# Kernel optimization log

Measured on AMD Instinct MI355X. Metric: run time of the kernel, lower is better.

## Reference

```python
import jax, jax.numpy as jnp
import numpy as np

STATE_LEN = 128
SEQ_LEN = 2048  # middle segment length; total T = SEQ_LEN + 2*STATE_LEN = 2304


def _l2norm(t):
    # matches torch F.normalize(p=2, dim=-1, eps=1e-12)
    n = jnp.sqrt(jnp.sum(t * t, axis=-1, keepdims=True))
    return t / jnp.maximum(n, 1e-12)


def setup_inputs() -> dict:
    key = jax.random.key(0)
    ks = jax.random.split(key, 8)
    B, D, H, dk, dv = 1, 1024, 16, 64, 64
    T = SEQ_LEN + 2 * STATE_LEN
    x = jax.random.normal(ks[0], (B, T, D), dtype=jnp.float32)
    w = lambda k, do: jax.random.normal(k, (H, D, do), dtype=jnp.float32) * 0.02
    return {
        "x": x,
        "Wq": w(ks[1], dk),
        "Wk": w(ks[2], dk),
        "Wv": w(ks[3], dv),
        "Wq_state": w(ks[4], dk),
        "Wk_state": w(ks[5], dk),
        "Wv_state": w(ks[6], dv),
        "scaling_factor": jnp.full((H,), 1.0 / np.sqrt(dk), dtype=jnp.float32),
    }


def reference(x, Wq, Wk, Wv, Wq_state, Wk_state, Wv_state, scaling_factor):
    sl, seq = STATE_LEN, SEQ_LEN
    # extract_state: [start_state | sequence | end_state]
    x0 = x[:, :sl]
    xm = x[:, sl:sl + seq]
    x1 = x[:, sl + seq:]

    proj = lambda t, W: jnp.einsum('bsd,hdk->bhsk', t, W)  # StackedLinear, no bias

    q = jnp.concatenate([_l2norm(proj(x0, Wq_state)), _l2norm(proj(xm, Wq)), _l2norm(proj(x1, Wq_state))], axis=2)
    k = jnp.concatenate([_l2norm(proj(x0, Wk_state)), _l2norm(proj(xm, Wk)), _l2norm(proj(x1, Wk_state))], axis=2)
    v = jnp.concatenate([_l2norm(proj(x0, Wv_state)), _l2norm(proj(xm, Wv)), _l2norm(proj(x1, Wv_state))], axis=2)

    T = q.shape[2]
    row = jnp.arange(T)[:, None]
    col = jnp.arange(T)[None, :]
    allowed = col <= row  # causal (tril, diagonal=0)
    # end-state rows may not attend to start-state cols (attn_bias[..., seq+sl:seq+2sl, :sl] = 0 before log)
    allowed = allowed & ~((row >= sl + seq) & (col < sl))
    mask = jnp.where(allowed, 0.0, -jnp.inf).astype(q.dtype)  # log of 0/1 tril

    # per-head learnable scale applied to q@k^T, then additive mask, softmax, @v
    scores = jnp.einsum('bhqd,bhkd->bhqk', q, k) * scaling_factor[None, :, None, None] + mask
    att = jax.nn.softmax(scores, axis=-1)
    return jnp.einsum('bhqk,bhkd->bhqd', att, v)
```

## Files before the change

### kernel.cpp

```cpp
#include <hip/hip_runtime.h>
#include <hip/hip_bf16.h>

#define T_TOT 2304
#define DDIM  1024
#define NH    16
#define DK    64
#define SLEN  128
#define SEQ   2048

typedef __bf16 bf16x8 __attribute__((ext_vector_type(8)));
typedef __bf16 bf16x4 __attribute__((ext_vector_type(4)));
typedef float  f32x4  __attribute__((ext_vector_type(4)));

__device__ __forceinline__ void async_copy16(const void* gsrc, void* ldst) {
  __builtin_amdgcn_global_load_lds(
      (const __attribute__((address_space(1))) void*)gsrc,
      (__attribute__((address_space(3))) void*)ldst, 16, 0, 0);
}

__global__ __launch_bounds__(256) void convert_kernel(
    const float* __restrict__ x,
    const float* __restrict__ Wq, const float* __restrict__ Wk,
    const float* __restrict__ Wv, const float* __restrict__ Wqs,
    const float* __restrict__ Wks, const float* __restrict__ Wvs,
    __bf16* __restrict__ xb, __bf16* __restrict__ Wt) {
  const int b = blockIdx.x;
  const int tid = threadIdx.x;
  if (b < 576) {
    const float4* xin = (const float4*)x;
#pragma unroll
    for (int it = 0; it < 4; ++it) {
      int idx4 = b * 1024 + it * 256 + tid;
      float4 v = xin[idx4];
      bf16x4 o;
      o[0] = (__bf16)v.x; o[1] = (__bf16)v.y; o[2] = (__bf16)v.z; o[3] = (__bf16)v.w;
      *(bf16x4*)(xb + (size_t)idx4 * 4) = o;
    }
    return;
  }
  __shared__ float tile[64 * 65];
  const int wb = b - 576;
  const int m  = wb >> 8;
  const int rem = wb & 255;
  const int h  = rem >> 4;
  const int dt = rem & 15;
  const int d0 = dt * 64;
  const float* Wsrc = (m == 0 ? Wq : m == 1 ? Wk : m == 2 ? Wv
                      : m == 3 ? Wqs : m == 4 ? Wks : Wvs) + (size_t)h * (DDIM * DK);
#pragma unroll
  for (int rr = 0; rr < 4; ++rr) {
    int drow = rr * 16 + (tid >> 4);
    int nc   = (tid & 15) * 4;
    float4 v = *(const float4*)(Wsrc + (size_t)(d0 + drow) * DK + nc);
    tile[(nc + 0) * 65 + drow] = v.x;
    tile[(nc + 1) * 65 + drow] = v.y;
    tile[(nc + 2) * 65 + drow] = v.z;
    tile[(nc + 3) * 65 + drow] = v.w;
  }
  __syncthreads();
  {
    int n  = tid >> 2;
    int rg = (tid & 3) * 16;
    __bf16* dst = Wt + (((size_t)(m * NH + h)) * DK + n) * DDIM + d0 + rg;
    bf16x8 o0, o1;
#pragma unroll
    for (int e = 0; e < 8; e++) o0[e] = (__bf16)tile[n * 65 + rg + e];
#pragma unroll
    for (int e = 0; e < 8; e++) o1[e] = (__bf16)tile[n * 65 + rg + 8 + e];
    *(bf16x8*)dst = o0;
    *(bf16x8*)(dst + 8) = o1;
  }
}

__global__ __launch_bounds__(256) void proj_kernel(
    const __bf16* __restrict__ xb, const __bf16* __restrict__ Wt,
    const float* __restrict__ scal,
    __bf16* __restrict__ qkv, __bf16* __restrict__ vt) {
  const int ntile = blockIdx.x;
  const int rt    = blockIdx.y;
  const int which = blockIdx.z;
  const int r0    = rt * 128;
  const int m     = (rt == 0 || rt == 17) ? which + 3 : which;

  __shared__ __bf16 Xs[128 * 64];
  __shared__ __bf16 Wsh[128 * 64];

  const int tid  = threadIdx.x;
  const int wave = tid >> 6, lane = tid & 63;
  const int quad = lane >> 4, lc = lane & 15;
  const int wr   = wave >> 1, wc = wave & 1;
  const int h    = ntile * 2 + wc;

  const __bf16* Wbase = Wt + ((size_t)m * NH) * (DK * DDIM) + (size_t)(ntile * 128) * DDIM;

  const f32x4 fz = {0.f, 0.f, 0.f, 0.f};
  f32x4 acc[4][4];
#pragma unroll
  for (int i = 0; i < 4; i++)
#pragma unroll
    for (int j = 0; j < 4; j++) acc[i][j] = fz;

  for (int k0 = 0; k0 < DDIM; k0 += 64) {
#pragma unroll
    for (int it = 0; it < 4; ++it) {
      int L = it * 256 + tid;
      int row = L >> 3, c = (L & 7) ^ ((L >> 3) & 7);
      async_copy16(xb + (size_t)(r0 + row) * DDIM + k0 + c * 8,
                   (char*)Xs + (size_t)(it * 256 + wave * 64) * 16);
    }
#pragma unroll
    for (int it = 0; it < 4; ++it) {
      int L = it * 256 + tid;
      int row = L >> 3, c = (L & 7) ^ ((L >> 3) & 7);
      async_copy16(Wbase + (size_t)row * DDIM + k0 + c * 8,
                   (char*)Wsh + (size_t)(it * 256 + wave * 64) * 16);
    }
    __syncthreads();
#pragma unroll
    for (int kk = 0; kk < 2; kk++) {
      bf16x8 afr[4], bfr[4];
#pragma unroll
      for (int i = 0; i < 4; i++) {
        int row = wr * 64 + i * 16 + lc;
        int ch  = (kk * 4 + quad) ^ (row & 7);
        afr[i] = *(const bf16x8*)(Xs + (row * 8 + ch) * 8);
      }
#pragma unroll
      for (int j = 0; j < 4; j++) {
        int row = wc * 64 + j * 16 + lc;
        int ch  = (kk * 4 + quad) ^ (row & 7);
        bfr[j] = *(const bf16x8*)(Wsh + (row * 8 + ch) * 8);
      }
#pragma unroll
      for (int i = 0; i < 4; i++)
#pragma unroll
        for (int j = 0; j < 4; j++)
          acc[i][j] = __builtin_amdgcn_mfma_f32_16x16x32_bf16(afr[i], bfr[j], acc[i][j], 0, 0, 0);
    }
    __syncthreads();
  }

  const float qscale = (which == 0) ? scal[h] * 1.44269504088896f : 1.0f;
  float inv4[4][4];
#pragma unroll
  for (int i = 0; i < 4; i++) {
#pragma unroll
    for (int r = 0; r < 4; r++) {
      float s = 0.f;
#pragma unroll
      for (int j = 0; j < 4; j++) { float v = acc[i][j][r]; s += v * v; }
#pragma unroll
      for (int off = 1; off < 16; off <<= 1) s += __shfl_xor(s, off, 64);
      inv4[i][r] = qscale / fmaxf(sqrtf(s), 1e-12f);
    }
  }
  if (which == 2) {
    __bf16* vtp = vt + (size_t)h * (DK * T_TOT);
#pragma unroll
    for (int i = 0; i < 4; i++) {
      int rowbase = r0 + wr * 64 + i * 16 + quad * 4;
#pragma unroll
      for (int j = 0; j < 4; j++) {
        bf16x4 o;
#pragma unroll
        for (int r = 0; r < 4; r++) o[r] = (__bf16)(acc[i][j][r] * inv4[i][r]);
        *(bf16x4*)(vtp + (size_t)(j * 16 + lc) * T_TOT + rowbase) = o;
      }
    }
  } else {
    __bf16* outp = qkv + ((size_t)(which * NH + h)) * ((size_t)T_TOT * DK);
#pragma unroll
    for (int i = 0; i < 4; i++)
#pragma unroll
      for (int r = 0; r < 4; r++) {
        int row = r0 + wr * 64 + i * 16 + quad * 4 + r;
#pragma unroll
        for (int j = 0; j < 4; j++)
          outp[(size_t)row * DK + j * 16 + lc] = (__bf16)(acc[i][j][r] * inv4[i][r]);
      }
  }
}

__global__ __launch_bounds__(256, 3) void attn_kernel(
    const __bf16* __restrict__ qkv, const __bf16* __restrict__ vt,
    float* __restrict__ Opart, float* __restrict__ Lpart) {
  const int b    = blockIdx.x;
  const int h    = b & 15;
  const int rest = b >> 4;
  const int qg   = 35 - (rest >> 1);
  const int si   = rest & 1;
  const int q0b  = qg * 64;
  const int tid  = threadIdx.x;
  const int wave = tid >> 6, lane = tid & 63;
  const int quad = lane >> 4, lc = lane & 15;

  const __bf16* qp = qkv + ((size_t)h) * ((size_t)T_TOT * DK);
  const __bf16* kp = qkv + ((size_t)(NH + h)) * ((size_t)T_TOT * DK);
  const __bf16* vp = vt + (size_t)h * (DK * T_TOT);

  __shared__ __align__(16) char smem[40960];
  __bf16* Ks = (__bf16*)smem;
  __bf16* Vs = (__bf16*)(smem + 16384);
  __bf16* Pw = (__bf16*)(smem + 32768) + wave * 1024;

  bf16x8 qf[2];
#pragma unroll
  for (int kk = 0; kk < 2; kk++)
    qf[kk] = *(const bf16x8*)(qp + (size_t)(q0b + wave * 16 + lc) * DK + kk * 32 + quad * 8);

  const f32x4 fz = {0.f, 0.f, 0.f, 0.f};
  f32x4 acc[4];
#pragma unroll
  for (int dt = 0; dt < 4; dt++) acc[dt] = fz;
  float lp = 0.f;

  const int jsAll = (q0b >= SLEN + SEQ) ? 2 : 0;
  const int n     = qg - jsAll + 1;
  const int half  = (n + 1) >> 1;
  const int j0    = jsAll + (si ? half : 0);
  const int j1    = si ? qg : (jsAll + half - 1);

  auto stage = [&](int j, int bufi) {
    const __bf16* kT = kp + (size_t)j * 64 * DK;
    __bf16* Kd = Ks + bufi * 4096;
    __bf16* Vd = Vs + bufi * 4096;
#pragma unroll
    for (int it = 0; it < 2; ++it) {
      int L = it * 256 + tid;
      int row = L >> 3, c = (L & 7) ^ (row & 7);
      async_copy16(kT + (size_t)row * DK + c * 8,
                   (char*)Kd + (size_t)(it * 256 + wave * 64) * 16);
    }
#pragma unroll
    for (int it = 0; it < 2; ++it) {
      int L = it * 256 + tid;
      int d = L >> 3, c = (L & 7) ^ (d & 7);
      async_copy16(vp + (size_t)d * T_TOT + j * 64 + c * 8,
                   (char*)Vd + (size_t)(it * 256 + wave * 64) * 16);
    }
  };

  int cur = 0;
  if (j0 <= j1) stage(j0, 0);

  for (int j = j0; j <= j1; ++j) {
    __syncthreads();
    if (j < j1) stage(j + 1, cur ^ 1);

    const __bf16* Kc = Ks + cur * 4096;
    const __bf16* Vc = Vs + cur * 4096;

    f32x4 s[4];
#pragma unroll
    for (int kvt = 0; kvt < 4; kvt++) {
      int row = kvt * 16 + lc;
      bf16x8 a0 = *(const bf16x8*)(Kc + (row * 8 + (quad ^ (lc & 7))) * 8);
      bf16x8 a1 = *(const bf16x8*)(Kc + (row * 8 + ((4 + quad) ^ (lc & 7))) * 8);
      f32x4 t = __builtin_amdgcn_mfma_f32_16x16x32_bf16(a0, qf[0], fz, 0, 0, 0);
      s[kvt]  = __builtin_amdgcn_mfma_f32_16x16x32_bf16(a1, qf[1], t, 0, 0, 0);
    }

    const bool diag = (j == qg);
#pragma unroll
    for (int kvt = 0; kvt < 4; kvt++) {
      if (diag) {
#pragma unroll
        for (int r = 0; r < 4; r++)
          if ((kvt * 16 + quad * 4 + r) > (wave * 16 + lc)) s[kvt][r] = -__builtin_inff();
      }
      bf16x4 pb;
#pragma unroll
      for (int r = 0; r < 4; r++) {
        float pe = exp2f(s[kvt][r]);
        lp += pe;
        pb[r] = (__bf16)pe;
      }
      int c = (kvt * 4 + quad) ^ ((lc & 7) << 1);
      *(bf16x4*)(Pw + lc * 64 + c * 4) = pb;
    }

    bf16x8 pB[2];
#pragma unroll
    for (int kk = 0; kk < 2; kk++)
      pB[kk] = *(const bf16x8*)(Pw + lc * 64 + ((kk * 8 + quad * 2) ^ ((lc & 7) << 1)) * 4);
#pragma unroll
    for (int dt = 0; dt < 4; dt++) {
      int row = dt * 16 + lc;
#pragma unroll
      for (int kk = 0; kk < 2; kk++) {
        bf16x8 vA = *(const bf16x8*)(Vc + (row * 8 + ((kk * 4 + quad) ^ (lc & 7))) * 8);
        acc[dt] = __builtin_amdgcn_mfma_f32_16x16x32_bf16(vA, pB[kk], acc[dt], 0, 0, 0);
      }
    }
    cur ^= 1;
  }

  lp += __shfl_xor(lp, 16, 64);
  lp += __shfl_xor(lp, 32, 64);
  if (lane < 16) Lpart[(size_t)b * 64 + wave * 16 + lane] = lp;

  __syncthreads();
  float* Ot = (float*)smem + wave * (16 * 68);
#pragma unroll
  for (int dt = 0; dt < 4; dt++)
#pragma unroll
    for (int r = 0; r < 4; r++)
      Ot[lc * 68 + dt * 16 + quad * 4 + r] = acc[dt][r];

  float* Ob = Opart + (size_t)b * 4096;
  const int q2 = lane >> 2, dsg = (lane & 3) * 16;
#pragma unroll
  for (int g = 0; g < 4; g++) {
    f32x4 v = *(const f32x4*)(&Ot[q2 * 68 + dsg + g * 4]);
    *(f32x4*)(&Ob[(size_t)(wave * 16 + q2) * 64 + dsg + g * 4]) = v;
  }
}

__global__ __launch_bounds__(256) void combine_kernel(
    const float* __restrict__ Opart, const float* __restrict__ Lpart,
    float* __restrict__ out) {
  const int b  = blockIdx.x;
  const int h  = b & 15;
  const int qg = b >> 4;
  const int b0 = (((35 - qg) * 2) << 4) | h;
  const int b1 = b0 + 16;
  const int tid = threadIdx.x;

  __shared__ float invl[64];
  if (tid < 64)
    invl[tid] = 1.0f / (Lpart[(size_t)b0 * 64 + tid] + Lpart[(size_t)b1 * 64 + tid]);
  __syncthreads();

  const float* O0 = Opart + (size_t)b0 * 4096;
  const float* O1 = Opart + (size_t)b1 * 4096;
  float* op = out + ((size_t)h * T_TOT + qg * 64) * DK;
#pragma unroll
  for (int it = 0; it < 4; ++it) {
    int i4 = it * 256 + tid;
    f32x4 a = *(const f32x4*)(&O0[i4 * 4]);
    f32x4 c = *(const f32x4*)(&O1[i4 * 4]);
    float iv = invl[i4 >> 4];
    f32x4 o;
#pragma unroll
    for (int r = 0; r < 4; r++) o[r] = (a[r] + c[r]) * iv;
    *(f32x4*)(&op[i4 * 4]) = o;
  }
}

extern "C" void kernel_launch(void* const* d_in, const int* in_sizes, int n_in,
                              void* d_out, int out_size, void* d_ws, size_t ws_size,
                              hipStream_t stream) {
  const float* x    = (const float*)d_in[0];
  const float* Wq   = (const float*)d_in[1];
  const float* Wk   = (const float*)d_in[2];
  const float* Wv   = (const float*)d_in[3];
  const float* Wqs  = (const float*)d_in[4];
  const float* Wks  = (const float*)d_in[5];
  const float* Wvs  = (const float*)d_in[6];
  const float* scal = (const float*)d_in[7];
  float* out = (float*)d_out;

  char* ws = (char*)d_ws;
  size_t off = 0;
  __bf16* xb    = (__bf16*)(ws + off); off += (size_t)T_TOT * DDIM * 2;
  __bf16* Wt    = (__bf16*)(ws + off); off += (size_t)6 * NH * DK * DDIM * 2;
  __bf16* qkv   = (__bf16*)(ws + off); off += (size_t)2 * NH * T_TOT * DK * 2;
  __bf16* vt    = (__bf16*)(ws + off); off += (size_t)NH * DK * T_TOT * 2;
  float*  Opart = (float*)(ws + off);  off += (size_t)1152 * 4096 * 4;
  float*  Lpart = (float*)(ws + off);

  convert_kernel<<<2112, 256, 0, stream>>>(x, Wq, Wk, Wv, Wqs, Wks, Wvs, xb, Wt);
  proj_kernel<<<dim3(8, 18, 3), 256, 0, stream>>>(xb, Wt, scal, qkv, vt);
  attn_kernel<<<dim3(1152), 256, 0, stream>>>(qkv, vt, Opart, Lpart);
  combine_kernel<<<dim3(576), 256, 0, stream>>>(Opart, Lpart, out);
}
```

Baseline: 145.1 us.

## Use 128-row query tiles, register-resident P, three-way KV split with fused last-block combine

```diff
diff --git a/kernel.cpp b/kernel.cpp
--- a/kernel.cpp
+++ b/kernel.cpp
@@ -18,15 +18,31 @@
       (__attribute__((address_space(3))) void*)ldst, 16, 0, 0);
 }
 
+__device__ __forceinline__ unsigned cvtpk(float a, float b) {
+  unsigned r;
+  asm("v_cvt_pk_bf16_f32 %0, %1, %2" : "=v"(r) : "v"(a), "v"(b));
+  return r;
+}
+__device__ __forceinline__ void perm32swap(unsigned& a, unsigned& b) {
+  asm volatile("v_permlane32_swap_b32 %0, %1" : "+v"(a), "+v"(b));
+}
+__device__ __forceinline__ void perm16swap(unsigned& a, unsigned& b) {
+  asm volatile("v_permlane16_swap_b32 %0, %1" : "+v"(a), "+v"(b));
+}
+
 __global__ __launch_bounds__(256) void convert_kernel(
     const float* __restrict__ x,
     const float* __restrict__ Wq, const float* __restrict__ Wk,
     const float* __restrict__ Wv, const float* __restrict__ Wqs,
     const float* __restrict__ Wks, const float* __restrict__ Wvs,
-    __bf16* __restrict__ xb, __bf16* __restrict__ Wt) {
+    __bf16* __restrict__ xb, __bf16* __restrict__ Wt, int* __restrict__ cnt) {
   const int b = blockIdx.x;
   const int tid = threadIdx.x;
   if (b < 576) {
+    if (b == 0) {
+      cnt[tid] = 0;
+      if (tid < 32) cnt[256 + tid] = 0;
+    }
     const float4* xin = (const float4*)x;
 #pragma unroll
     for (int it = 0; it < 4; ++it) {
@@ -183,167 +199,186 @@
 
 __global__ __launch_bounds__(256, 3) void attn_kernel(
     const __bf16* __restrict__ qkv, const __bf16* __restrict__ vt,
-    float* __restrict__ Opart, float* __restrict__ Lpart) {
+    float* __restrict__ Opart, float* __restrict__ Lpart,
+    int* __restrict__ cnt, float* __restrict__ out) {
   const int b    = blockIdx.x;
-  const int h    = b & 15;
-  const int rest = b >> 4;
-  const int qg   = 35 - (rest >> 1);
-  const int si   = rest & 1;
-  const int q0b  = qg * 64;
+  const int qg2  = 17 - (b / 48);
+  const int r48  = b % 48;
+  const int si   = r48 >> 4;
+  const int h    = r48 & 15;
+  const int q0b  = qg2 * 128;
   const int tid  = threadIdx.x;
   const int wave = tid >> 6, lane = tid & 63;
   const int quad = lane >> 4, lc = lane & 15;
 
-  const __bf16* qp = qkv + ((size_t)h) * ((size_t)T_TOT * DK);
-  const __bf16* kp = qkv + ((size_t)(NH + h)) * ((size_t)T_TOT * DK);
+  const __bf16* qp = qkv + (size_t)h * ((size_t)T_TOT * DK);
+  const __bf16* kp = qkv + (size_t)(NH + h) * ((size_t)T_TOT * DK);
   const __bf16* vp = vt + (size_t)h * (DK * T_TOT);
 
-  __shared__ __align__(16) char smem[40960];
-  __bf16* Ks = (__bf16*)smem;
-  __bf16* Vs = (__bf16*)(smem + 16384);
-  __bf16* Pw = (__bf16*)(smem + 32768) + wave * 1024;
-
-  bf16x8 qf[2];
-#pragma unroll
-  for (int kk = 0; kk < 2; kk++)
-    qf[kk] = *(const bf16x8*)(qp + (size_t)(q0b + wave * 16 + lc) * DK + kk * 32 + quad * 8);
+  __shared__ __align__(16) __bf16 Ks[2][4096];
+  __shared__ __align__(16) __bf16 Vs[2][4096];
+  __shared__ float invl[128];
+  __shared__ int lastFlag;
+
+  bf16x8 qf[2][2];
+  const int qrow = q0b + wave * 32 + lc;
+#pragma unroll
+  for (int qt = 0; qt < 2; qt++)
+#pragma unroll
+    for (int kk = 0; kk < 2; kk++)
+      qf[qt][kk] = *(const bf16x8*)(qp + (size_t)(qrow + qt * 16) * DK + kk * 32 + quad * 8);
 
   const f32x4 fz = {0.f, 0.f, 0.f, 0.f};
-  f32x4 acc[4];
-#pragma unroll
-  for (int dt = 0; dt < 4; dt++) acc[dt] = fz;
-  float lp = 0.f;
-
-  const int jsAll = (q0b >= SLEN + SEQ) ? 2 : 0;
-  const int n     = qg - jsAll + 1;
-  const int half  = (n + 1) >> 1;
-  const int j0    = jsAll + (si ? half : 0);
-  const int j1    = si ? qg : (jsAll + half - 1);
+  f32x4 acc[2][4];
+#pragma unroll
+  for (int qt = 0; qt < 2; qt++)
+#pragma unroll
+    for (int dt = 0; dt < 4; dt++) acc[qt][dt] = fz;
+  float lp[2] = {0.f, 0.f};
+
+  const int js   = (qg2 == 17) ? 2 : 0;
+  const int jmax = 2 * qg2 + 1;
+  const int n    = jmax - js + 1;
+  const int base = n / 3, rem = n % 3;
+  const int j0   = js + si * base + (si < rem ? si : rem);
+  const int j1   = j0 + base + (si < rem ? 1 : 0) - 1;
 
   auto stage = [&](int j, int bufi) {
     const __bf16* kT = kp + (size_t)j * 64 * DK;
-    __bf16* Kd = Ks + bufi * 4096;
-    __bf16* Vd = Vs + bufi * 4096;
 #pragma unroll
     for (int it = 0; it < 2; ++it) {
       int L = it * 256 + tid;
       int row = L >> 3, c = (L & 7) ^ (row & 7);
       async_copy16(kT + (size_t)row * DK + c * 8,
-                   (char*)Kd + (size_t)(it * 256 + wave * 64) * 16);
+                   (char*)&Ks[bufi][0] + (size_t)(it * 256 + wave * 64) * 16);
     }
 #pragma unroll
     for (int it = 0; it < 2; ++it) {
       int L = it * 256 + tid;
       int d = L >> 3, c = (L & 7) ^ (d & 7);
       async_copy16(vp + (size_t)d * T_TOT + j * 64 + c * 8,
-                   (char*)Vd + (size_t)(it * 256 + wave * 64) * 16);
+                   (char*)&Vs[bufi][0] + (size_t)(it * 256 + wave * 64) * 16);
     }
   };
 
   int cur = 0;
   if (j0 <= j1) stage(j0, 0);
+
+  const int qmaxw = q0b + wave * 32 + 31;
 
   for (int j = j0; j <= j1; ++j) {
     __syncthreads();
     if (j < j1) stage(j + 1, cur ^ 1);
 
-    const __bf16* Kc = Ks + cur * 4096;
-    const __bf16* Vc = Vs + cur * 4096;
-
-    f32x4 s[4];
-#pragma unroll
-    for (int kvt = 0; kvt < 4; kvt++) {
-      int row = kvt * 16 + lc;
-      bf16x8 a0 = *(const bf16x8*)(Kc + (row * 8 + (quad ^ (lc & 7))) * 8);
-      bf16x8 a1 = *(const bf16x8*)(Kc + (row * 8 + ((4 + quad) ^ (lc & 7))) * 8);
-      f32x4 t = __builtin_amdgcn_mfma_f32_16x16x32_bf16(a0, qf[0], fz, 0, 0, 0);
-      s[kvt]  = __builtin_amdgcn_mfma_f32_16x16x32_bf16(a1, qf[1], t, 0, 0, 0);
-    }
-
-    const bool diag = (j == qg);
-#pragma unroll
-    for (int kvt = 0; kvt < 4; kvt++) {
-      if (diag) {
-#pragma unroll
-        for (int r = 0; r < 4; r++)
-          if ((kvt * 16 + quad * 4 + r) > (wave * 16 + lc)) s[kvt][r] = -__builtin_inff();
+    if (64 * j <= qmaxw) {
+      const __bf16* Kc = &Ks[cur][0];
+      const __bf16* Vc = &Vs[cur][0];
+      const bool diagw = (64 * j + 63 > q0b + wave * 32);
+
+#pragma unroll
+      for (int hp = 0; hp < 2; hp++) {
+        f32x4 s[2][2];
+        __builtin_amdgcn_s_setprio(1);
+#pragma unroll
+        for (int kl = 0; kl < 2; kl++) {
+          int row = (hp * 2 + kl) * 16 + lc;
+          bf16x8 a0 = *(const bf16x8*)(Kc + (row * 8 + (quad ^ (lc & 7))) * 8);
+          bf16x8 a1 = *(const bf16x8*)(Kc + (row * 8 + ((4 + quad) ^ (lc & 7))) * 8);
+#pragma unroll
+          for (int qt = 0; qt < 2; qt++) {
+            f32x4 t = __builtin_amdgcn_mfma_f32_16x16x32_bf16(a0, qf[qt][0], fz, 0, 0, 0);
+            s[kl][qt] = __builtin_amdgcn_mfma_f32_16x16x32_bf16(a1, qf[qt][1], t, 0, 0, 0);
+          }
+        }
+        __builtin_amdgcn_s_setprio(0);
+
+        bf16x8 pA[2];
+#pragma unroll
+        for (int qt = 0; qt < 2; qt++) {
+          unsigned cw[2][2];
+#pragma unroll
+          for (int kl = 0; kl < 2; kl++) {
+            float pe[4];
+#pragma unroll
+            for (int rr = 0; rr < 4; rr++) {
+              float v = exp2f(s[kl][qt][rr]);
+              if (diagw) {
+                int kvg = 64 * j + (hp * 2 + kl) * 16 + quad * 4 + rr;
+                if (kvg > q0b + wave * 32 + qt * 16 + lc) v = 0.f;
+              }
+              lp[qt] += v;
+              pe[rr] = v;
+            }
+            cw[kl][0] = cvtpk(pe[0], pe[1]);
+            cw[kl][1] = cvtpk(pe[2], pe[3]);
+          }
+          unsigned w0 = cw[0][0], x0 = cw[1][0];
+          perm32swap(w0, x0); perm16swap(w0, x0);
+          unsigned w1 = cw[0][1], x1 = cw[1][1];
+          perm32swap(w1, x1); perm16swap(w1, x1);
+          union { unsigned u[4]; bf16x8 v; } pu;
+          pu.u[0] = w0; pu.u[1] = w1; pu.u[2] = x0; pu.u[3] = x1;
+          pA[qt] = pu.v;
+        }
+
+        __builtin_amdgcn_s_setprio(1);
+#pragma unroll
+        for (int dt = 0; dt < 4; dt++) {
+          int row = dt * 16 + lc;
+          bf16x8 vB = *(const bf16x8*)(Vc + (row * 8 + ((hp * 4 + quad) ^ (lc & 7))) * 8);
+#pragma unroll
+          for (int qt = 0; qt < 2; qt++)
+            acc[qt][dt] = __builtin_amdgcn_mfma_f32_16x16x32_bf16(pA[qt], vB, acc[qt][dt], 0, 0, 0);
+        }
+        __builtin_amdgcn_s_setprio(0);
       }
-      bf16x4 pb;
-#pragma unroll
-      for (int r = 0; r < 4; r++) {
-        float pe = exp2f(s[kvt][r]);
-        lp += pe;
-        pb[r] = (__bf16)pe;
-      }
-      int c = (kvt * 4 + quad) ^ ((lc & 7) << 1);
-      *(bf16x4*)(Pw + lc * 64 + c * 4) = pb;
-    }
-
-    bf16x8 pB[2];
-#pragma unroll
-    for (int kk = 0; kk < 2; kk++)
-      pB[kk] = *(const bf16x8*)(Pw + lc * 64 + ((kk * 8 + quad * 2) ^ ((lc & 7) << 1)) * 4);
-#pragma unroll
-    for (int dt = 0; dt < 4; dt++) {
-      int row = dt * 16 + lc;
-#pragma unroll
-      for (int kk = 0; kk < 2; kk++) {
-        bf16x8 vA = *(const bf16x8*)(Vc + (row * 8 + ((kk * 4 + quad) ^ (lc & 7))) * 8);
-        acc[dt] = __builtin_amdgcn_mfma_f32_16x16x32_bf16(vA, pB[kk], acc[dt], 0, 0, 0);
-      }
     }
     cur ^= 1;
   }
 
-  lp += __shfl_xor(lp, 16, 64);
-  lp += __shfl_xor(lp, 32, 64);
-  if (lane < 16) Lpart[(size_t)b * 64 + wave * 16 + lane] = lp;
-
+  float* Ob = Opart + (size_t)b * 8192;
+#pragma unroll
+  for (int qt = 0; qt < 2; qt++) {
+    float l = lp[qt];
+    l += __shfl_xor(l, 16, 64);
+    l += __shfl_xor(l, 32, 64);
+    if (lane < 16) Lpart[(size_t)b * 128 + wave * 32 + qt * 16 + lane] = l;
+#pragma unroll
+    for (int dt = 0; dt < 4; dt++)
+#pragma unroll
+      for (int rr = 0; rr < 4; rr++)
+        Ob[(size_t)(wave * 32 + qt * 16 + quad * 4 + rr) * 64 + dt * 16 + lc] = acc[qt][dt][rr];
+  }
+
+  __threadfence();
   __syncthreads();
-  float* Ot = (float*)smem + wave * (16 * 68);
-#pragma unroll
-  for (int dt = 0; dt < 4; dt++)
-#pragma unroll
-    for (int r = 0; r < 4; r++)
-      Ot[lc * 68 + dt * 16 + quad * 4 + r] = acc[dt][r];
-
-  float* Ob = Opart + (size_t)b * 4096;
-  const int q2 = lane >> 2, dsg = (lane & 3) * 16;
-#pragma unroll
-  for (int g = 0; g < 4; g++) {
-    f32x4 v = *(const f32x4*)(&Ot[q2 * 68 + dsg + g * 4]);
-    *(f32x4*)(&Ob[(size_t)(wave * 16 + q2) * 64 + dsg + g * 4]) = v;
-  }
-}
-
-__global__ __launch_bounds__(256) void combine_kernel(
-    const float* __restrict__ Opart, const float* __restrict__ Lpart,
-    float* __restrict__ out) {
-  const int b  = blockIdx.x;
-  const int h  = b & 15;
-  const int qg = b >> 4;
-  const int b0 = (((35 - qg) * 2) << 4) | h;
-  const int b1 = b0 + 16;
-  const int tid = threadIdx.x;
-
-  __shared__ float invl[64];
-  if (tid < 64)
-    invl[tid] = 1.0f / (Lpart[(size_t)b0 * 64 + tid] + Lpart[(size_t)b1 * 64 + tid]);
+  if (tid == 0) lastFlag = (atomicAdd(&cnt[qg2 * 16 + h], 1) == 2);
   __syncthreads();
-
-  const float* O0 = Opart + (size_t)b0 * 4096;
-  const float* O1 = Opart + (size_t)b1 * 4096;
-  float* op = out + ((size_t)h * T_TOT + qg * 64) * DK;
-#pragma unroll
-  for (int it = 0; it < 4; ++it) {
+  if (!lastFlag) return;
+  __threadfence();
+
+  const int bb = (17 - qg2) * 48 + h;
+  const float* O0 = Opart + (size_t)bb * 8192;
+  const float* O1 = O0 + (size_t)16 * 8192;
+  const float* O2 = O0 + (size_t)32 * 8192;
+  const float* L0 = Lpart + (size_t)bb * 128;
+  const float* L1 = L0 + (size_t)16 * 128;
+  const float* L2 = L0 + (size_t)32 * 128;
+  if (tid < 128) invl[tid] = 1.0f / (L0[tid] + L1[tid] + L2[tid]);
+  __syncthreads();
+
+  float* op = out + ((size_t)h * T_TOT + q0b) * DK;
+#pragma unroll
+  for (int it = 0; it < 8; ++it) {
     int i4 = it * 256 + tid;
-    f32x4 a = *(const f32x4*)(&O0[i4 * 4]);
-    f32x4 c = *(const f32x4*)(&O1[i4 * 4]);
+    f32x4 a = *(const f32x4*)(O0 + (size_t)i4 * 4);
+    f32x4 c = *(const f32x4*)(O1 + (size_t)i4 * 4);
+    f32x4 d = *(const f32x4*)(O2 + (size_t)i4 * 4);
     float iv = invl[i4 >> 4];
     f32x4 o;
 #pragma unroll
-    for (int r = 0; r < 4; r++) o[r] = (a[r] + c[r]) * iv;
-    *(f32x4*)(&op[i4 * 4]) = o;
+    for (int r = 0; r < 4; r++) o[r] = (a[r] + c[r] + d[r]) * iv;
+    *(f32x4*)(op + (size_t)i4 * 4) = o;
   }
 }
 
@@ -366,11 +401,11 @@
   __bf16* Wt    = (__bf16*)(ws + off); off += (size_t)6 * NH * DK * DDIM * 2;
   __bf16* qkv   = (__bf16*)(ws + off); off += (size_t)2 * NH * T_TOT * DK * 2;
   __bf16* vt    = (__bf16*)(ws + off); off += (size_t)NH * DK * T_TOT * 2;
-  float*  Opart = (float*)(ws + off);  off += (size_t)1152 * 4096 * 4;
-  float*  Lpart = (float*)(ws + off);
-
-  convert_kernel<<<2112, 256, 0, stream>>>(x, Wq, Wk, Wv, Wqs, Wks, Wvs, xb, Wt);
+  float*  Opart = (float*)(ws + off);  off += (size_t)864 * 8192 * 4;
+  float*  Lpart = (float*)(ws + off);  off += (size_t)864 * 128 * 4;
+  int*    cnt   = (int*)(ws + off);    off += (size_t)288 * 4;
+
+  convert_kernel<<<2112, 256, 0, stream>>>(x, Wq, Wk, Wv, Wqs, Wks, Wvs, xb, Wt, cnt);
   proj_kernel<<<dim3(8, 18, 3), 256, 0, stream>>>(xb, Wt, scal, qkv, vt);
-  attn_kernel<<<dim3(1152), 256, 0, stream>>>(qkv, vt, Opart, Lpart);
-  combine_kernel<<<dim3(576), 256, 0, stream>>>(Opart, Lpart, out);
-}
+  attn_kernel<<<dim3(864), 256, 0, stream>>>(qkv, vt, Opart, Lpart, cnt, out);
+}
```

Measured after the change: 285.8 us. 97.0% more time.
